# Kernel tuning notes

Measured on AMD Instinct MI355X. Metric: run time of the kernel, lower is better.

Reference implementation:

```python
import jax, jax.numpy as jnp
import numpy as np

N = 100000
E = 3200000
NFEAT = 256
NHID = 128
NCLASS = 64


def setup_inputs() -> dict:
    key = jax.random.key(0)
    ks = jax.random.split(key, 10)
    x = jax.random.normal(ks[0], (N, NFEAT), dtype=jnp.float32)
    src = jax.random.randint(ks[1], (E,), 0, N, dtype=jnp.int32).astype(jnp.int64)
    dst = jax.random.randint(ks[2], (E,), 0, N, dtype=jnp.int32).astype(jnp.int64)
    # Glorot-ish init for GraphConv weights
    def w(k, i, o):
        return jax.random.normal(k, (i, o), dtype=jnp.float32) * (1.0 / np.sqrt(i))
    W0 = w(ks[3], NFEAT, NHID)
    b0 = jnp.zeros((NHID,), dtype=jnp.float32)
    W1 = w(ks[4], NHID, NHID)
    b1 = jnp.zeros((NHID,), dtype=jnp.float32)
    W2 = w(ks[5], NHID, NCLASS)
    b2 = jnp.zeros((NCLASS,), dtype=jnp.float32)
    return {"x": x, "src": src, "dst": dst,
            "W0": W0, "b0": b0, "W1": W1, "b1": b1, "W2": W2, "b2": b2}


def _degree_norms(src, dst, dtype):
    ones = jnp.ones(src.shape, dtype)
    deg_out = jax.ops.segment_sum(ones, src, num_segments=N)
    deg_in = jax.ops.segment_sum(ones, dst, num_segments=N)
    # clamp zero degrees to avoid inf (DGL clamps to 1)
    n_src = jnp.where(deg_out > 0, deg_out, 1.0) ** -0.5
    n_dst = jnp.where(deg_in > 0, deg_in, 1.0) ** -0.5
    return n_src, n_dst


def _graph_conv(h, src, dst, n_src, n_dst, W, b):
    # weight first (math-equivalent to DGL ordering), then normalized SpMM
    h = h @ W                              # [N, out]
    msg = h[src] * n_src[src][:, None]     # [E, out] gather + src norm
    agg = jax.ops.segment_sum(msg, dst, num_segments=N)  # [N, out]
    return agg * n_dst[:, None] + b


def reference(x, src, dst, W0, b0, W1, b1, W2, b2):
    n_src, n_dst = _degree_norms(src, dst, x.dtype)
    h = _graph_conv(x, src, dst, n_src, n_dst, W0, b0)
    # dropout is identity in eval mode
    h = _graph_conv(h, src, dst, n_src, n_dst, W1, b1)
    h = _graph_conv(h, src, dst, n_src, n_dst, W2, b2)
    return jax.nn.softmax(h, axis=1)
```

## Files before the change

### kernel.cpp

```cpp
#include <hip/hip_runtime.h>
#include <hip/hip_bf16.h>

#define N_NODES 100000
#define N_EDGES 3200000
#define NFEAT 256
#define NHID 128
#define NCLASS 64
#define SCAN_B 1024
#define NB_SCAN ((N_NODES + SCAN_B - 1) / SCAN_B)
#define NVEC4 (N_EDGES / 4)
#define RANGE (N_NODES / 8)
#define NSL 64

typedef unsigned int uint32;
typedef unsigned short ushort16;
typedef __attribute__((ext_vector_type(8))) short bf16x8;
typedef __attribute__((ext_vector_type(4))) float f32x4;
typedef __attribute__((ext_vector_type(2))) float f32x2;

static __device__ __forceinline__ float b2f(ushort16 u) {
    union { float f; uint32 i; } c; c.i = ((uint32)u) << 16; return c.f;
}
static __device__ __forceinline__ ushort16 f2b(float f) {
    union { float f; uint32 i; } c; c.f = f;
    uint32 r = (c.i + 0x7FFFu + ((c.i >> 16) & 1u)) >> 16;
    return (ushort16)r;
}
static __device__ __forceinline__ float blo(uint32 u) {
    union { float f; uint32 i; } c; c.i = u << 16; return c.f;
}
static __device__ __forceinline__ float bhi(uint32 u) {
    union { float f; uint32 i; } c; c.i = u & 0xFFFF0000u; return c.f;
}
static __device__ __forceinline__ uint32 pack2(float a, float b) {
    return (uint32)f2b(a) | ((uint32)f2b(b) << 16);
}

__global__ __launch_bounds__(512) void k_hist(const int4* __restrict__ src4,
                                              const int4* __restrict__ dst4,
                                              uint32* __restrict__ scratch) {
    __shared__ uint32 h[RANGE];
    int g = blockIdx.x & 7, sl = blockIdx.x >> 3;
    int lo = g * RANGE, hi = lo + RANGE;
    for (int i = threadIdx.x; i < RANGE; i += 512) h[i] = 0u;
    __syncthreads();
    for (int t = sl * 512 + threadIdx.x; t < NVEC4; t += NSL * 512) {
        int4 s = src4[t], d = dst4[t];
        if (s.x >= lo && s.x < hi) atomicAdd(&h[s.x - lo], 1u);
        if (s.y >= lo && s.y < hi) atomicAdd(&h[s.y - lo], 1u);
        if (s.z >= lo && s.z < hi) atomicAdd(&h[s.z - lo], 1u);
        if (s.w >= lo && s.w < hi) atomicAdd(&h[s.w - lo], 1u);
        if (d.x >= lo && d.x < hi) atomicAdd(&h[d.x - lo], 65536u);
        if (d.y >= lo && d.y < hi) atomicAdd(&h[d.y - lo], 65536u);
        if (d.z >= lo && d.z < hi) atomicAdd(&h[d.z - lo], 65536u);
        if (d.w >= lo && d.w < hi) atomicAdd(&h[d.w - lo], 65536u);
    }
    __syncthreads();
    uint32* dstp = scratch + ((size_t)(g * NSL + sl)) * RANGE;
    for (int i = threadIdx.x; i < RANGE; i += 512) dstp[i] = h[i];
}

__global__ void k_sumdeg(const uint32* __restrict__ scratch, int* __restrict__ deg_in,
                         float* __restrict__ n_src, float* __restrict__ n_dst) {
    int i = blockIdx.x * blockDim.x + threadIdx.x;
    if (i >= N_NODES) return;
    if (i == 0) n_src[N_NODES] = 0.f;
    int g = i / RANGE, r = i - g * RANGE;
    const uint32* base = scratch + (size_t)g * NSL * RANGE + r;
    uint32 so = 0, di = 0;
    for (int s = 0; s < NSL; s++) {
        uint32 v = base[(size_t)s * RANGE];
        so += v & 0xFFFFu;
        di += v >> 16;
    }
    deg_in[i] = (int)di;
    uint32 so1 = so < 1u ? 1u : so;
    uint32 di1 = di < 1u ? 1u : di;
    n_src[i] = rsqrtf((float)so1);
    n_dst[i] = rsqrtf((float)di1);
}

__global__ void k_scan1(const int* __restrict__ deg_in, int* __restrict__ row_ptr,
                        int* __restrict__ blk_sums) {
    __shared__ int sh[SCAN_B];
    int i = blockIdx.x * SCAN_B + threadIdx.x;
    int v = (i < N_NODES) ? deg_in[i] : 0;
    sh[threadIdx.x] = v;
    __syncthreads();
    for (int o = 1; o < SCAN_B; o <<= 1) {
        int t = 0;
        if ((int)threadIdx.x >= o) t = sh[threadIdx.x - o];
        __syncthreads();
        sh[threadIdx.x] += t;
        __syncthreads();
    }
    if (i < N_NODES) row_ptr[i] = sh[threadIdx.x] - v;
    if (threadIdx.x == SCAN_B - 1) blk_sums[blockIdx.x] = sh[SCAN_B - 1];
}

__global__ void k_scan2(int* __restrict__ blk_sums) {
    if (threadIdx.x == 0 && blockIdx.x == 0) {
        int acc = 0;
        for (int b = 0; b < NB_SCAN; b++) { int v = blk_sums[b]; blk_sums[b] = acc; acc += v; }
        blk_sums[NB_SCAN] = acc;
    }
}

__global__ void k_scan3(const int* __restrict__ blk_sums, int* __restrict__ row_ptr) {
    int i = blockIdx.x * SCAN_B + threadIdx.x;
    if (i < N_NODES) row_ptr[i] += blk_sums[blockIdx.x];
    if (i == 0) row_ptr[N_NODES] = blk_sums[NB_SCAN];
}

__global__ void k_offsets(uint32* __restrict__ scratch, const int* __restrict__ row_ptr) {
    int i = blockIdx.x * blockDim.x + threadIdx.x;
    if (i >= N_NODES) return;
    int g = i / RANGE, r = i - g * RANGE;
    uint32* base = scratch + (size_t)g * NSL * RANGE + r;
    uint32 run = (uint32)row_ptr[i];
    for (int s = 0; s < NSL; s++) {
        uint32 v = base[(size_t)s * RANGE];
        base[(size_t)s * RANGE] = run;
        run += v >> 16;
    }
}

__global__ __launch_bounds__(512) void k_fill2(const int4* __restrict__ src4,
                                               const int4* __restrict__ dst4,
                                               const uint32* __restrict__ scratch,
                                               int* __restrict__ col) {
    __shared__ uint32 cur[RANGE];
    int g = blockIdx.x & 7, sl = blockIdx.x >> 3;
    int lo = g * RANGE, hi = lo + RANGE;
    const uint32* base = scratch + ((size_t)(g * NSL + sl)) * RANGE;
    for (int i = threadIdx.x; i < RANGE; i += 512) cur[i] = base[i];
    __syncthreads();
    for (int t = sl * 512 + threadIdx.x; t < NVEC4; t += NSL * 512) {
        int4 s = src4[t], d = dst4[t];
        if (d.x >= lo && d.x < hi) { uint32 p = atomicAdd(&cur[d.x - lo], 1u); col[p] = s.x; }
        if (d.y >= lo && d.y < hi) { uint32 p = atomicAdd(&cur[d.y - lo], 1u); col[p] = s.y; }
        if (d.z >= lo && d.z < hi) { uint32 p = atomicAdd(&cur[d.z - lo], 1u); col[p] = s.z; }
        if (d.w >= lo && d.w < hi) { uint32 p = atomicAdd(&cur[d.w - lo], 1u); col[p] = s.w; }
    }
}

__global__ void k_w01(const float* __restrict__ W0, const float* __restrict__ W1,
                      float* __restrict__ W01) {
    __shared__ float row[NHID];
    int r = blockIdx.x, c = threadIdx.x;
    row[c] = W0[r * NHID + c];
    __syncthreads();
    float acc = 0.f;
    for (int k = 0; k < NHID; k++) acc += row[k] * W1[k * NHID + c];
    W01[r * NHID + c] = acc;
}

__global__ void k_wc(const float* __restrict__ W01, const float* __restrict__ W2,
                     float* __restrict__ Wc, ushort16* __restrict__ Wt) {
    __shared__ float row[NHID];
    int r = blockIdx.x, c = threadIdx.x;
    row[c] = W01[r * NHID + c];
    row[c + 64] = W01[r * NHID + c + 64];
    __syncthreads();
    float acc = 0.f;
    for (int k = 0; k < NHID; k++) acc += row[k] * W2[k * NCLASS + c];
    Wc[r * NCLASS + c] = acc;
    Wt[(size_t)c * NFEAT + r] = f2b(acc);
}

__global__ void k_bv(const float* __restrict__ b0, const float* __restrict__ W1,
                     const float* __restrict__ b1, const float* __restrict__ W2,
                     float* __restrict__ bv) {
    __shared__ float tmp[NHID];
    int c = threadIdx.x;
    for (int cc = c; cc < NHID; cc += 64) {
        float a = 0.f;
        for (int k = 0; k < NHID; k++) a += b0[k] * W1[k * NHID + cc];
        tmp[cc] = a;
    }
    __syncthreads();
    float a1 = 0.f, a2 = 0.f;
    for (int k = 0; k < NHID; k++) {
        float wv = W2[k * NCLASS + c];
        a1 += tmp[k] * wv;
        a2 += b1[k] * wv;
    }
    bv[c] = a1;
    bv[64 + c] = a2;
}

__global__ __launch_bounds__(256) void k_gemm_y(const float* __restrict__ x,
                                                const ushort16* __restrict__ Wt,
                                                const float* __restrict__ n_src,
                                                ushort16* __restrict__ y) {
    int tid = threadIdx.x;
    int wid = tid >> 6, lane = tid & 63;
    int q = lane >> 4, r = lane & 15;
    int rowbase = blockIdx.x * 64 + wid * 16;
    int rowld = min(rowbase + r, N_NODES - 1);
    const float* xp = x + (size_t)rowld * NFEAT + q * 8;

    float4 alo[8], ahi[8];
#pragma unroll
    for (int kt = 0; kt < 8; kt++) {
        alo[kt] = *(const float4*)(xp + kt * 32);
        ahi[kt] = *(const float4*)(xp + kt * 32 + 4);
    }

    f32x4 acc0 = {0.f, 0.f, 0.f, 0.f};
    f32x4 acc1 = {0.f, 0.f, 0.f, 0.f};
    f32x4 acc2 = {0.f, 0.f, 0.f, 0.f};
    f32x4 acc3 = {0.f, 0.f, 0.f, 0.f};

#pragma unroll
    for (int kt = 0; kt < 8; kt++) {
        bf16x8 af;
        af[0] = (short)f2b(alo[kt].x); af[1] = (short)f2b(alo[kt].y);
        af[2] = (short)f2b(alo[kt].z); af[3] = (short)f2b(alo[kt].w);
        af[4] = (short)f2b(ahi[kt].x); af[5] = (short)f2b(ahi[kt].y);
        af[6] = (short)f2b(ahi[kt].z); af[7] = (short)f2b(ahi[kt].w);
        const int ko = kt * 32 + q * 8;
        bf16x8 b0 = *(const bf16x8*)(Wt + (size_t)(0 * 16 + r) * NFEAT + ko);
        bf16x8 b1 = *(const bf16x8*)(Wt + (size_t)(1 * 16 + r) * NFEAT + ko);
        bf16x8 b2 = *(const bf16x8*)(Wt + (size_t)(2 * 16 + r) * NFEAT + ko);
        bf16x8 b3 = *(const bf16x8*)(Wt + (size_t)(3 * 16 + r) * NFEAT + ko);
        acc0 = __builtin_amdgcn_mfma_f32_16x16x32_bf16(af, b0, acc0, 0, 0, 0);
        acc1 = __builtin_amdgcn_mfma_f32_16x16x32_bf16(af, b1, acc1, 0, 0, 0);
        acc2 = __builtin_amdgcn_mfma_f32_16x16x32_bf16(af, b2, acc2, 0, 0, 0);
        acc3 = __builtin_amdgcn_mfma_f32_16x16x32_bf16(af, b3, acc3, 0, 0, 0);
    }

    int srow0 = rowbase + q * 4;
#pragma unroll
    for (int i = 0; i < 4; i++) {
        int rr = srow0 + i;
        if (rr < N_NODES) {
            float ns = n_src[rr];
            ushort16* yp = y + (size_t)rr * NCLASS + r;
            yp[0]  = f2b(acc0[i] * ns);
            yp[16] = f2b(acc1[i] * ns);
            yp[32] = f2b(acc2[i] * ns);
            yp[48] = f2b(acc3[i] * ns);
        } else if (rr == N_NODES) {
            ushort16* yp = y + (size_t)rr * NCLASS + r;
            yp[0] = 0; yp[16] = 0; yp[32] = 0; yp[48] = 0;
        }
    }
}

template <int PASS>
__global__ __launch_bounds__(256) void k_agg(
        const int* __restrict__ row_ptr, const int* __restrict__ col,
        const float* __restrict__ wsrc,
        const float* __restrict__ n_src, const float* __restrict__ n_dst,
        const ushort16* __restrict__ in, ushort16* __restrict__ out,
        float* __restrict__ outf,
        float* __restrict__ tsave, float* __restrict__ tssave,
        const float* __restrict__ t1, const float* __restrict__ t2,
        const float* __restrict__ bv, const float* __restrict__ b2) {
    int wid = threadIdx.x >> 6, lane = threadIdx.x & 63;
    int node = blockIdx.x * 4 + wid;
    if (node > N_NODES) return;
    int g = lane >> 3, sub = lane & 7;

    if (node == N_NODES) {
        if (PASS != 3) {
            if (g == 0) {
                uint4 z = {0u, 0u, 0u, 0u};
                *((uint4*)((char*)out + ((size_t)N_NODES << 7)) + sub) = z;
            }
            if (lane == 0) {
                tsave[N_NODES] = 0.f;
                if (PASS == 1) tssave[N_NODES] = 0.f;
            }
        }
        return;
    }

    int s = row_ptr[node], e = row_ptr[node + 1];
    const char* inb = (const char*)in;
    const char* wb  = (const char*)wsrc;
    uint32 subo = (uint32)sub << 4;

    f32x2 a0 = {0.f, 0.f}, a1 = {0.f, 0.f}, a2 = {0.f, 0.f}, a3 = {0.f, 0.f};
    float accs = 0.f;

#define CH(P)                                                                  \
    {                                                                          \
        int p_ = (P);                                                          \
        bool v_ = p_ < e;                                                      \
        int j_ = v_ ? col[p_] : N_NODES;                                       \
        uint32 fo_ = ((uint32)j_ << 7) + subo;                                 \
        uint4 u_ = *(const uint4*)(inb + fo_);                                 \
        if (PASS != 3) accs += *(const float*)(wb + ((uint32)j_ << 2));        \
        f32x2 q0; q0.x = blo(u_.x); q0.y = bhi(u_.x);                          \
        f32x2 q1; q1.x = blo(u_.y); q1.y = bhi(u_.y);                          \
        f32x2 q2; q2.x = blo(u_.z); q2.y = bhi(u_.z);                          \
        f32x2 q3; q3.x = blo(u_.w); q3.y = bhi(u_.w);                          \
        a0 += q0; a1 += q1; a2 += q2; a3 += q3;                                \
    }

    for (int base = s; base < e; base += 32) {
        CH(base + g)
        CH(base + 8 + g)
        CH(base + 16 + g)
        CH(base + 24 + g)
    }
#undef CH

#pragma unroll
    for (int off = 8; off <= 32; off <<= 1) {
        a0.x += __shfl_xor(a0.x, off, 64); a0.y += __shfl_xor(a0.y, off, 64);
        a1.x += __shfl_xor(a1.x, off, 64); a1.y += __shfl_xor(a1.y, off, 64);
        a2.x += __shfl_xor(a2.x, off, 64); a2.y += __shfl_xor(a2.y, off, 64);
        a3.x += __shfl_xor(a3.x, off, 64); a3.y += __shfl_xor(a3.y, off, 64);
        if (PASS != 3) accs += __shfl_xor(accs, off, 64);
    }

    float nd = n_dst[node];
    if (PASS == 3) {
        float t2n = t2[node], t1n = t1[node];
        const float* bvA = bv + sub * 8;
        const float* bvB = bv + 64 + sub * 8;
        const float* b2p = b2 + sub * 8;
        float v0 = a0.x * nd + t2n * bvA[0] + t1n * bvB[0] + b2p[0];
        float v1 = a0.y * nd + t2n * bvA[1] + t1n * bvB[1] + b2p[1];
        float v2 = a1.x * nd + t2n * bvA[2] + t1n * bvB[2] + b2p[2];
        float v3 = a1.y * nd + t2n * bvA[3] + t1n * bvB[3] + b2p[3];
        float v4 = a2.x * nd + t2n * bvA[4] + t1n * bvB[4] + b2p[4];
        float v5 = a2.y * nd + t2n * bvA[5] + t1n * bvB[5] + b2p[5];
        float v6 = a3.x * nd + t2n * bvA[6] + t1n * bvB[6] + b2p[6];
        float v7 = a3.y * nd + t2n * bvA[7] + t1n * bvB[7] + b2p[7];
        float m = fmaxf(fmaxf(fmaxf(v0, v1), fmaxf(v2, v3)),
                        fmaxf(fmaxf(v4, v5), fmaxf(v6, v7)));
#pragma unroll
        for (int off = 1; off <= 4; off <<= 1) m = fmaxf(m, __shfl_xor(m, off, 64));
        float e0 = __expf(v0 - m), e1 = __expf(v1 - m), e2 = __expf(v2 - m), e3 = __expf(v3 - m);
        float e4 = __expf(v4 - m), e5 = __expf(v5 - m), e6 = __expf(v6 - m), e7 = __expf(v7 - m);
        float sum = ((e0 + e1) + (e2 + e3)) + ((e4 + e5) + (e6 + e7));
#pragma unroll
        for (int off = 1; off <= 4; off <<= 1) sum += __shfl_xor(sum, off, 64);
        float r = 1.0f / sum;
        if (g == 0) {
            float4 o0 = {e0 * r, e1 * r, e2 * r, e3 * r};
            float4 o1 = {e4 * r, e5 * r, e6 * r, e7 * r};
            float4* op = (float4*)(outf + (size_t)node * NCLASS + sub * 8);
            op[0] = o0;
            op[1] = o1;
        }
    } else {
        if (g == 0) {
            float sc = nd * n_src[node];
            uint32 w0 = pack2(a0.x * sc, a0.y * sc);
            uint32 w1 = pack2(a1.x * sc, a1.y * sc);
            uint32 w2 = pack2(a2.x * sc, a2.y * sc);
            uint32 w3 = pack2(a3.x * sc, a3.y * sc);
            uint4 w = {w0, w1, w2, w3};
            *((uint4*)((char*)out + ((size_t)node << 7)) + sub) = w;
        }
        if (lane == 0) {
            float T = accs * nd;
            tsave[node] = T;
            if (PASS == 1) tssave[node] = T * n_src[node];
        }
    }
}

extern "C" void kernel_launch(void* const* d_in, const int* in_sizes, int n_in,
                              void* d_out, int out_size, void* d_ws, size_t ws_size,
                              hipStream_t stream) {
    const float* x   = (const float*)d_in[0];
    const int*   src = (const int*)d_in[1];
    const int*   dst = (const int*)d_in[2];
    const float* W0  = (const float*)d_in[3];
    const float* b0  = (const float*)d_in[4];
    const float* W1  = (const float*)d_in[5];
    const float* b1  = (const float*)d_in[6];
    const float* W2  = (const float*)d_in[7];
    const float* b2  = (const float*)d_in[8];
    float* out = (float*)d_out;

    size_t off = 0;
    auto alloc = [&](size_t bytes) {
        void* p = (char*)d_ws + off;
        off = (off + bytes + 255) & ~(size_t)255;
        return p;
    };
    int*      deg_in   = (int*)alloc(N_NODES * 4);
    float*    n_src    = (float*)alloc((N_NODES + 1) * 4);
    float*    n_dst    = (float*)alloc(N_NODES * 4);
    int*      row_ptr  = (int*)alloc((N_NODES + 1) * 4);
    int*      blk_sums = (int*)alloc((NB_SCAN + 1) * 4);
    int*      col      = (int*)alloc((size_t)N_EDGES * 4);
    uint32*   scratch  = (uint32*)alloc((size_t)8 * NSL * RANGE * 4);
    float*    W01      = (float*)alloc(NFEAT * NHID * 4);
    float*    Wc       = (float*)alloc(NFEAT * NCLASS * 4);
    ushort16* Wt       = (ushort16*)alloc((size_t)NFEAT * NCLASS * 2);
    float*    bv       = (float*)alloc(128 * 4);
    float*    t1       = (float*)alloc((N_NODES + 1) * 4);
    float*    t1s      = (float*)alloc((N_NODES + 1) * 4);
    float*    t2       = (float*)alloc((N_NODES + 1) * 4);
    ushort16* bufB1    = (ushort16*)alloc((size_t)(N_NODES + 1) * NCLASS * 2);
    ushort16* bufB2    = (ushort16*)alloc((size_t)(N_NODES + 1) * NCLASS * 2);
    (void)ws_size; (void)in_sizes; (void)n_in; (void)out_size;

    const int TB = 256;
    const int NBn = (N_NODES + TB - 1) / TB;
    const int NW = (N_NODES + 3) / 4 + 1;
    const int GP = 8 * NSL;

    k_hist<<<GP, 512, 0, stream>>>((const int4*)src, (const int4*)dst, scratch);
    k_sumdeg<<<NBn, TB, 0, stream>>>(scratch, deg_in, n_src, n_dst);
    k_scan1<<<NB_SCAN, SCAN_B, 0, stream>>>(deg_in, row_ptr, blk_sums);
    k_scan2<<<1, 64, 0, stream>>>(blk_sums);
    k_scan3<<<NB_SCAN, SCAN_B, 0, stream>>>(blk_sums, row_ptr);
    k_offsets<<<NBn, TB, 0, stream>>>(scratch, row_ptr);
    k_fill2<<<GP, 512, 0, stream>>>((const int4*)src, (const int4*)dst, scratch, col);

    k_w01<<<NFEAT, NHID, 0, stream>>>(W0, W1, W01);
    k_wc<<<NFEAT, NCLASS, 0, stream>>>(W01, W2, Wc, Wt);
    k_bv<<<1, NCLASS, 0, stream>>>(b0, W1, b1, W2, bv);

    k_gemm_y<<<(N_NODES + 64) / 64, 256, 0, stream>>>(x, Wt, n_src, bufB1);

    k_agg<1><<<NW, 256, 0, stream>>>(row_ptr, col, n_src, n_src, n_dst, bufB1, bufB2,
                                     nullptr, t1, t1s, nullptr, nullptr, nullptr, nullptr);
    k_agg<2><<<NW, 256, 0, stream>>>(row_ptr, col, t1s, n_src, n_dst, bufB2, bufB1,
                                     nullptr, t2, nullptr, nullptr, nullptr, nullptr, nullptr);
    k_agg<3><<<NW, 256, 0, stream>>>(row_ptr, col, nullptr, n_src, n_dst, bufB1, nullptr,
                                     out, nullptr, nullptr, t1, t2, bv, b2);
}
```

Measured before the change: 524.3 us.

## Replace range-partitioned LDS histogram CSR build with global atomic degree and fill

Swaps the LDS-based, range-partitioned degree histogram and slice-offset CSR construction for direct global atomics on per-node degree and cursor arrays. This removes the 8x redundant reads of src/dst, the large scratch buffer and the offsets pass. In exchange, every edge now does a global atomic, and the fill order within a row becomes nondeterministic.

```diff
diff --git a/kernel.cpp b/kernel.cpp
--- a/kernel.cpp
+++ b/kernel.cpp
@@ -9,8 +9,6 @@
 #define SCAN_B 1024
 #define NB_SCAN ((N_NODES + SCAN_B - 1) / SCAN_B)
 #define NVEC4 (N_EDGES / 4)
-#define RANGE (N_NODES / 8)
-#define NSL 64
 
 typedef unsigned int uint32;
 typedef unsigned short ushort16;
@@ -36,48 +34,33 @@
     return (uint32)f2b(a) | ((uint32)f2b(b) << 16);
 }
 
-__global__ __launch_bounds__(512) void k_hist(const int4* __restrict__ src4,
-                                              const int4* __restrict__ dst4,
-                                              uint32* __restrict__ scratch) {
-    __shared__ uint32 h[RANGE];
-    int g = blockIdx.x & 7, sl = blockIdx.x >> 3;
-    int lo = g * RANGE, hi = lo + RANGE;
-    for (int i = threadIdx.x; i < RANGE; i += 512) h[i] = 0u;
-    __syncthreads();
-    for (int t = sl * 512 + threadIdx.x; t < NVEC4; t += NSL * 512) {
+__global__ void k_zero(int* __restrict__ deg_out, int* __restrict__ deg_in) {
+    int i = blockIdx.x * blockDim.x + threadIdx.x;
+    if (i < N_NODES) { deg_out[i] = 0; deg_in[i] = 0; }
+}
+
+__global__ __launch_bounds__(256) void k_deg(const int4* __restrict__ src4,
+                                             const int4* __restrict__ dst4,
+                                             int* __restrict__ deg_out,
+                                             int* __restrict__ deg_in) {
+    int stride = gridDim.x * 256;
+    for (int t = blockIdx.x * 256 + threadIdx.x; t < NVEC4; t += stride) {
         int4 s = src4[t], d = dst4[t];
-        if (s.x >= lo && s.x < hi) atomicAdd(&h[s.x - lo], 1u);
-        if (s.y >= lo && s.y < hi) atomicAdd(&h[s.y - lo], 1u);
-        if (s.z >= lo && s.z < hi) atomicAdd(&h[s.z - lo], 1u);
-        if (s.w >= lo && s.w < hi) atomicAdd(&h[s.w - lo], 1u);
-        if (d.x >= lo && d.x < hi) atomicAdd(&h[d.x - lo], 65536u);
-        if (d.y >= lo && d.y < hi) atomicAdd(&h[d.y - lo], 65536u);
-        if (d.z >= lo && d.z < hi) atomicAdd(&h[d.z - lo], 65536u);
-        if (d.w >= lo && d.w < hi) atomicAdd(&h[d.w - lo], 65536u);
-    }
-    __syncthreads();
-    uint32* dstp = scratch + ((size_t)(g * NSL + sl)) * RANGE;
-    for (int i = threadIdx.x; i < RANGE; i += 512) dstp[i] = h[i];
-}
-
-__global__ void k_sumdeg(const uint32* __restrict__ scratch, int* __restrict__ deg_in,
-                         float* __restrict__ n_src, float* __restrict__ n_dst) {
+        atomicAdd(&deg_out[s.x], 1); atomicAdd(&deg_out[s.y], 1);
+        atomicAdd(&deg_out[s.z], 1); atomicAdd(&deg_out[s.w], 1);
+        atomicAdd(&deg_in[d.x], 1);  atomicAdd(&deg_in[d.y], 1);
+        atomicAdd(&deg_in[d.z], 1);  atomicAdd(&deg_in[d.w], 1);
+    }
+}
+
+__global__ void k_norm(const int* __restrict__ deg_out, const int* __restrict__ deg_in,
+                       float* __restrict__ n_src, float* __restrict__ n_dst) {
     int i = blockIdx.x * blockDim.x + threadIdx.x;
     if (i >= N_NODES) return;
     if (i == 0) n_src[N_NODES] = 0.f;
-    int g = i / RANGE, r = i - g * RANGE;
-    const uint32* base = scratch + (size_t)g * NSL * RANGE + r;
-    uint32 so = 0, di = 0;
-    for (int s = 0; s < NSL; s++) {
-        uint32 v = base[(size_t)s * RANGE];
-        so += v & 0xFFFFu;
-        di += v >> 16;
-    }
-    deg_in[i] = (int)di;
-    uint32 so1 = so < 1u ? 1u : so;
-    uint32 di1 = di < 1u ? 1u : di;
-    n_src[i] = rsqrtf((float)so1);
-    n_dst[i] = rsqrtf((float)di1);
+    int so = deg_out[i], di = deg_in[i];
+    n_src[i] = rsqrtf((float)(so < 1 ? 1 : so));
+    n_dst[i] = rsqrtf((float)(di < 1 ? 1 : di));
 }
 
 __global__ void k_scan1(const int* __restrict__ deg_in, int* __restrict__ row_ptr,
@@ -106,41 +89,28 @@
     }
 }
 
-__global__ void k_scan3(const int* __restrict__ blk_sums, int* __restrict__ row_ptr) {
+__global__ void k_scan3(const int* __restrict__ blk_sums, int* __restrict__ row_ptr,
+                        int* __restrict__ cur) {
     int i = blockIdx.x * SCAN_B + threadIdx.x;
-    if (i < N_NODES) row_ptr[i] += blk_sums[blockIdx.x];
+    if (i < N_NODES) {
+        int v = row_ptr[i] + blk_sums[blockIdx.x];
+        row_ptr[i] = v;
+        cur[i] = v;
+    }
     if (i == 0) row_ptr[N_NODES] = blk_sums[NB_SCAN];
 }
 
-__global__ void k_offsets(uint32* __restrict__ scratch, const int* __restrict__ row_ptr) {
-    int i = blockIdx.x * blockDim.x + threadIdx.x;
-    if (i >= N_NODES) return;
-    int g = i / RANGE, r = i - g * RANGE;
-    uint32* base = scratch + (size_t)g * NSL * RANGE + r;
-    uint32 run = (uint32)row_ptr[i];
-    for (int s = 0; s < NSL; s++) {
-        uint32 v = base[(size_t)s * RANGE];
-        base[(size_t)s * RANGE] = run;
-        run += v >> 16;
-    }
-}
-
-__global__ __launch_bounds__(512) void k_fill2(const int4* __restrict__ src4,
-                                               const int4* __restrict__ dst4,
-                                               const uint32* __restrict__ scratch,
-                                               int* __restrict__ col) {
-    __shared__ uint32 cur[RANGE];
-    int g = blockIdx.x & 7, sl = blockIdx.x >> 3;
-    int lo = g * RANGE, hi = lo + RANGE;
-    const uint32* base = scratch + ((size_t)(g * NSL + sl)) * RANGE;
-    for (int i = threadIdx.x; i < RANGE; i += 512) cur[i] = base[i];
-    __syncthreads();
-    for (int t = sl * 512 + threadIdx.x; t < NVEC4; t += NSL * 512) {
+__global__ __launch_bounds__(256) void k_fill(const int4* __restrict__ src4,
+                                              const int4* __restrict__ dst4,
+                                              int* __restrict__ cur,
+                                              int* __restrict__ col) {
+    int stride = gridDim.x * 256;
+    for (int t = blockIdx.x * 256 + threadIdx.x; t < NVEC4; t += stride) {
         int4 s = src4[t], d = dst4[t];
-        if (d.x >= lo && d.x < hi) { uint32 p = atomicAdd(&cur[d.x - lo], 1u); col[p] = s.x; }
-        if (d.y >= lo && d.y < hi) { uint32 p = atomicAdd(&cur[d.y - lo], 1u); col[p] = s.y; }
-        if (d.z >= lo && d.z < hi) { uint32 p = atomicAdd(&cur[d.z - lo], 1u); col[p] = s.z; }
-        if (d.w >= lo && d.w < hi) { uint32 p = atomicAdd(&cur[d.w - lo], 1u); col[p] = s.w; }
+        int p0 = atomicAdd(&cur[d.x], 1); col[p0] = s.x;
+        int p1 = atomicAdd(&cur[d.y], 1); col[p1] = s.y;
+        int p2 = atomicAdd(&cur[d.z], 1); col[p2] = s.z;
+        int p3 = atomicAdd(&cur[d.w], 1); col[p3] = s.w;
     }
 }
 
@@ -386,13 +356,14 @@
         off = (off + bytes + 255) & ~(size_t)255;
         return p;
     };
+    int*      deg_out  = (int*)alloc(N_NODES * 4);
     int*      deg_in   = (int*)alloc(N_NODES * 4);
     float*    n_src    = (float*)alloc((N_NODES + 1) * 4);
     float*    n_dst    = (float*)alloc(N_NODES * 4);
     int*      row_ptr  = (int*)alloc((N_NODES + 1) * 4);
+    int*      cursor   = (int*)alloc(N_NODES * 4);
     int*      blk_sums = (int*)alloc((NB_SCAN + 1) * 4);
     int*      col      = (int*)alloc((size_t)N_EDGES * 4);
-    uint32*   scratch  = (uint32*)alloc((size_t)8 * NSL * RANGE * 4);
     float*    W01      = (float*)alloc(NFEAT * NHID * 4);
     float*    Wc       = (float*)alloc(NFEAT * NCLASS * 4);
     ushort16* Wt       = (ushort16*)alloc((size_t)NFEAT * NCLASS * 2);
@@ -407,15 +378,15 @@
     const int TB = 256;
     const int NBn = (N_NODES + TB - 1) / TB;
     const int NW = (N_NODES + 3) / 4 + 1;
-    const int GP = 8 * NSL;
-
-    k_hist<<<GP, 512, 0, stream>>>((const int4*)src, (const int4*)dst, scratch);
-    k_sumdeg<<<NBn, TB, 0, stream>>>(scratch, deg_in, n_src, n_dst);
+    const int GS = 2048;
+
+    k_zero<<<NBn, TB, 0, stream>>>(deg_out, deg_in);
+    k_deg<<<GS, TB, 0, stream>>>((const int4*)src, (const int4*)dst, deg_out, deg_in);
+    k_norm<<<NBn, TB, 0, stream>>>(deg_out, deg_in, n_src, n_dst);
     k_scan1<<<NB_SCAN, SCAN_B, 0, stream>>>(deg_in, row_ptr, blk_sums);
     k_scan2<<<1, 64, 0, stream>>>(blk_sums);
-    k_scan3<<<NB_SCAN, SCAN_B, 0, stream>>>(blk_sums, row_ptr);
-    k_offsets<<<NBn, TB, 0, stream>>>(scratch, row_ptr);
-    k_fill2<<<GP, 512, 0, stream>>>((const int4*)src, (const int4*)dst, scratch, col);
+    k_scan3<<<NB_SCAN, SCAN_B, 0, stream>>>(blk_sums, row_ptr, cursor);
+    k_fill<<<GS, TB, 0, stream>>>((const int4*)src, (const int4*)dst, cursor, col);
 
     k_w01<<<NFEAT, NHID, 0, stream>>>(W0, W1, W01);
     k_wc<<<NFEAT, NCLASS, 0, stream>>>(W01, W2, Wc, Wt);
```

Result: slower. 918.4 us (+75.1%).
